# Performance work log

Hardware: AMD Instinct MI355X
Metric: run time of the kernel (lower is better)

Reference implementation:

```python
import jax, jax.numpy as jnp
import numpy as np
import math

B = 65536
N_NUM = 64; N_CAT = 16; CAT_SIZE = 1000; EMB = 16
ND = 64; NA = 64; OUT = ND + NA; NSTEPS = 5; GAMMA = 1.5
NFEAT = N_NUM + N_CAT * EMB          # 320
NGROUPS = N_NUM + N_CAT              # 80
GROUP_IDX = np.repeat(np.arange(NGROUPS), [1] * N_NUM + [EMB] * N_CAT)  # len 320
RES_SCALE = math.sqrt(0.5)
BN_EPS = 1e-5


def setup_inputs() -> dict:
    keys = iter(jax.random.split(jax.random.key(0), 64))
    def rn(shape, std):
        return jax.random.normal(next(keys), shape, jnp.float32) * std
    def mk_bn(c, lead=()):
        # stacked (scale, bias, running_mean, running_var) along axis -2
        s = 1.0 + 0.05 * jax.random.normal(next(keys), (*lead, c), jnp.float32)
        b = 0.05 * jax.random.normal(next(keys), (*lead, c), jnp.float32)
        m = 0.05 * jax.random.normal(next(keys), (*lead, c), jnp.float32)
        v = 1.0 + 0.1 * jax.random.uniform(next(keys), (*lead, c), dtype=jnp.float32)
        return jnp.stack([s, b, m, v], axis=-2)
    inp = {}
    inp["x_num"] = jax.random.normal(next(keys), (B, N_NUM), jnp.float32)
    inp["x_cat"] = jax.random.randint(next(keys), (B, N_CAT), 0, CAT_SIZE)
    inp["emb_W"] = rn((N_CAT, CAT_SIZE, EMB), 0.1)
    inp["in_bn"] = mk_bn(NFEAT)
    inp["sh_W0"] = rn((NFEAT, 2 * OUT), 1.0 / math.sqrt(NFEAT))
    inp["sh_b0"] = jnp.zeros((2 * OUT,), jnp.float32)
    inp["sh_bn0"] = mk_bn(2 * OUT)
    inp["sh_W1"] = rn((OUT, 2 * OUT), 1.0 / math.sqrt(OUT))
    inp["sh_b1"] = jnp.zeros((2 * OUT,), jnp.float32)
    inp["sh_bn1"] = mk_bn(2 * OUT)
    inp["init_W"] = rn((2, OUT, 2 * OUT), 1.0 / math.sqrt(OUT))
    inp["init_b"] = jnp.zeros((2, 2 * OUT), jnp.float32)
    inp["init_bn"] = mk_bn(2 * OUT, (2,))
    inp["step_W"] = rn((NSTEPS, 2, OUT, 2 * OUT), 1.0 / math.sqrt(OUT))
    inp["step_b"] = jnp.zeros((NSTEPS, 2, 2 * OUT), jnp.float32)
    inp["step_bn"] = mk_bn(2 * OUT, (NSTEPS, 2))
    inp["att_W"] = rn((NSTEPS, NA, NGROUPS), 1.0 / math.sqrt(NA))
    inp["att_b"] = jnp.zeros((NSTEPS, NGROUPS), jnp.float32)
    inp["att_bn"] = mk_bn(NGROUPS, (NSTEPS,))
    inp["out_W"] = rn((ND, 1), 1.0 / math.sqrt(ND))
    inp["out_b"] = jnp.zeros((1,), jnp.float32)
    return inp


def bn_apply(x, p):
    s, b, m, v = p  # each [C]
    return (x - m) * jax.lax.rsqrt(v + BN_EPS) * s + b


def glu_layer(x, W, b, bn):
    h = bn_apply(x @ W + b, bn)          # [B, 2*OUT]
    o, g = jnp.split(h, 2, axis=1)
    return o * jax.nn.sigmoid(g)


def glu_block(x, W, b, bn):
    y = glu_layer(x, W, b, bn)
    return (x + y) * RES_SCALE if x.shape == y.shape else y


def sparsemax(z):
    # along axis=1; Martins & Astudillo 2016
    zs = -jnp.sort(-z, axis=1)
    cs = jnp.cumsum(zs, axis=1)
    r = jnp.arange(1, z.shape[1] + 1, dtype=z.dtype)
    support = (1.0 + r * zs) > cs
    k = jnp.maximum(support.sum(axis=1, keepdims=True), 1)
    cs_k = jnp.take_along_axis(cs, k - 1, axis=1)
    tau = (cs_k - 1.0) / k.astype(z.dtype)
    return jnp.maximum(z - tau, 0.0)


def _forward(x_num, x_cat, emb_W, in_bn, sh_W0, sh_b0, sh_bn0, sh_W1, sh_b1, sh_bn1,
             init_W, init_b, init_bn, step_W, step_b, step_bn, att_W, att_b, att_bn,
             out_W, out_b):
    # categorical embeddings: [B, N_CAT, EMB] -> [B, N_CAT*EMB]
    emb = emb_W[np.arange(N_CAT)[None, :], x_cat].reshape(x_cat.shape[0], -1)
    x = jnp.concatenate([x_num, emb], axis=1)  # [B, NFEAT]
    x = bn_apply(x, in_bn)

    def ft_shared(h):
        h = glu_block(h, sh_W0, sh_b0, sh_bn0)   # 320 -> 128, no residual
        return glu_block(h, sh_W1, sh_b1, sh_bn1)  # residual

    def ft_indep(h, W, b, bn):
        for i in range(W.shape[0]):
            h = glu_block(h, W[i], b[i], bn[i])
        return h

    out0 = ft_indep(ft_shared(x), init_W, init_b, init_bn)
    a = out0[:, ND:]
    prior = jnp.ones((x.shape[0], NGROUPS), x.dtype)
    decision_sum = jnp.zeros((x.shape[0], ND), x.dtype)
    for step in range(NSTEPS):
        logits = bn_apply(a @ att_W[step] + att_b[step], att_bn[step]) * prior
        mask_group = sparsemax(logits)           # [B, NGROUPS]
        prior = prior * (GAMMA - mask_group)
        mask = mask_group[:, GROUP_IDX]          # [B, NFEAT] (repeat_interleave)
        out = ft_indep(ft_shared(mask * x), step_W[step], step_b[step], step_bn[step])
        d, a = out[:, :ND], out[:, ND:]
        decision_sum = decision_sum + jax.nn.relu(d)
    return decision_sum @ out_W + out_b          # [B, 1]


def reference(x_num, x_cat, emb_W, in_bn, sh_W0, sh_b0, sh_bn0, sh_W1, sh_b1, sh_bn1,
              init_W, init_b, init_bn, step_W, step_b, step_bn, att_W, att_b, att_bn,
              out_W, out_b):
    return _forward(x_num, x_cat, emb_W, in_bn, sh_W0, sh_b0, sh_bn0, sh_W1, sh_b1,
                    sh_bn1, init_W, init_b, init_bn, step_W, step_b, step_bn,
                    att_W, att_b, att_bn, out_W, out_b)
```

## Files before the change

### kernel.cpp

```cpp
#include <hip/hip_runtime.h>
#include <math.h>
#include <stdint.h>

typedef _Float16 half_t;
typedef _Float16 half8 __attribute__((ext_vector_type(8)));
typedef __fp16 fp16x2 __attribute__((ext_vector_type(2)));
typedef float floatx4 __attribute__((ext_vector_type(4)));
typedef float floatx16 __attribute__((ext_vector_type(16)));

constexpr float BN_EPS_C = 1e-5f;
constexpr float RES_SCALE_C = 0.70710678118654752f;
constexpr float GAMMA_C = 1.5f;
#define B_TOT 65536

__device__ __forceinline__ uint32_t pack2(float y) {
    const half_t h = (half_t)y;
    const half_t l = (half_t)(y - (float)h);
    union { half_t f; unsigned short u; } a, b; a.f = h; b.f = l;
    return (uint32_t)a.u | ((uint32_t)b.u << 16);
}
__device__ __forceinline__ void unpack2(uint32_t v, half_t& h, half_t& l) {
    union { unsigned short u; half_t f; } a, b;
    a.u = (unsigned short)(v & 0xffffu); b.u = (unsigned short)(v >> 16);
    h = a.f; l = b.f;
}
__device__ __forceinline__ void split_pair(float y0, float y1, half_t& h0, half_t& l0, half_t& h1, half_t& l1) {
    fp16x2 hh = __builtin_amdgcn_cvt_pkrtz(y0, y1);
    fp16x2 ll = __builtin_amdgcn_cvt_pkrtz(y0 - (float)hh.x, y1 - (float)hh.y);
    h0 = (half_t)hh.x; l0 = (half_t)ll.x; h1 = (half_t)hh.y; l1 = (half_t)ll.y;
}
__device__ __forceinline__ void pack2_pair(float y0, float y1, uint32_t& w0, uint32_t& w1) {
    fp16x2 hh = __builtin_amdgcn_cvt_pkrtz(y0, y1);
    fp16x2 ll = __builtin_amdgcn_cvt_pkrtz(y0 - (float)hh.x, y1 - (float)hh.y);
    const uint32_t hb = __builtin_bit_cast(uint32_t, hh);
    const uint32_t lb = __builtin_bit_cast(uint32_t, ll);
    w0 = (hb & 0xffffu) | (lb << 16);
    w1 = (hb >> 16) | (lb & 0xffff0000u);
}

__global__ void wsplit_kernel(const float* __restrict__ sh_W0, const float* __restrict__ sh_W1,
                              const float* __restrict__ init_W, const float* __restrict__ step_W,
                              half_t* __restrict__ Wh, half_t* __restrict__ Wl)
{
    const int b = blockIdx.x, n = threadIdx.x;
    const float* src; int k; size_t base;
    if (b < 320)      { src = sh_W0;           k = b;       base = 0; }
    else if (b < 448) { src = sh_W1;           k = b - 320; base = 81920; }
    else if (b < 576) { src = init_W;          k = b - 448; base = 114688; }
    else if (b < 704) { src = init_W + 32768;  k = b - 576; base = 147456; }
    else {
        int j = (b - 704) >> 7; k = (b - 704) & 127;
        src = step_W + (size_t)j * 32768; base = 180224 + (size_t)j * 32768;
    }
    const float v = src[k * 256 + n];
    const half_t hi = (half_t)v;
    const half_t lo = (half_t)(v - (float)hi);
    const size_t idx = base + (size_t)(((k >> 3) * 256 + n) * 8 + (k & 7));
    Wh[idx] = hi; Wl[idx] = lo;
}

__global__ void wsplit_att_kernel(const float* __restrict__ att_W,
                                  half_t* __restrict__ aWh, half_t* __restrict__ aWl)
{
    const int b = blockIdx.x;
    const int n = threadIdx.x;
    const int step = b >> 6, k = b & 63;
    const float v = att_W[(size_t)b * 80 + n];
    const half_t h = (half_t)v;
    const half_t l = (half_t)(v - (float)h);
    const size_t idx = (size_t)step * 5120 + (size_t)(((k >> 3) * 80 + n) * 8 + (k & 7));
    aWh[idx] = h; aWl[idx] = l;
}

__global__ void embed_bn_kernel(const float* __restrict__ x_num, const int* __restrict__ x_cat,
                                const float* __restrict__ emb_W, const float* __restrict__ in_bn,
                                uint32_t* __restrict__ xp)
{
    const int idx = blockIdx.x * 256 + threadIdx.x;
    const int s = idx / 320, j = idx - s * 320;
    float v;
    if (j < 64) v = x_num[(size_t)s * 64 + j];
    else {
        const int c = (j - 64) >> 4, e = (j - 64) & 15;
        v = emb_W[(size_t)(c * 1000 + x_cat[(size_t)s * 16 + c]) * 16 + e];
    }
    const float val = (v - in_bn[640 + j]) * (in_bn[j] * __frsqrt_rn(in_bn[960 + j] + BN_EPS_C)) + in_bn[320 + j];
    xp[idx] = pack2(val);
}

__device__ __forceinline__ void bn_fold(const float* __restrict__ bn, const float* __restrict__ bias,
                                        int c, float& sc, float& sh)
{
    sc = bn[c] * __frsqrt_rn(bn[768 + c] + BN_EPS_C);
    sh = fmaf(bias[c] - bn[512 + c], sc, bn[256 + c]);
}

__device__ __forceinline__ float glu_val(float accO, float accG,
                                         float sc_o, float sh_o, float sc_g, float sh_g)
{
    const float o = fmaf(accO, sc_o, sh_o);
    const float g = fmaf(accG, sc_g, sh_g);
    const float e = __expf(-g);
    return o * __builtin_amdgcn_rcpf(1.f + e);
}

#define MFMA32(A, B, C) C = __builtin_amdgcn_mfma_f32_32x32x16_f16(A, B, C, 0, 0, 0)
#define MFMA16(A, B, C) C = __builtin_amdgcn_mfma_f32_16x16x32_f16(A, B, C, 0, 0, 0)

__device__ __forceinline__ void layer_accum(const half_t (*H_h)[136], const half_t (*H_l)[136],
                                            const half_t* __restrict__ Wh, const half_t* __restrict__ Wl,
                                            size_t off, int n32, int k8, int no, int rot,
                                            floatx16* accO, floatx16* accG)
{
#pragma unroll 2
    for (int s = 0; s < 8; ++s) {
        const int sl8 = (s + rot) & 7;
        const int kq = sl8 * 2 + k8;
        const size_t wo = off + (size_t)(kq * 256 + no + n32) * 8;
        const half8 bo_h = *(const half8*)(Wh + wo);
        const half8 bo_l = *(const half8*)(Wl + wo);
        const half8 bg_h = *(const half8*)(Wh + wo + 1024);
        const half8 bg_l = *(const half8*)(Wl + wo + 1024);
#pragma unroll
        for (int mt = 0; mt < 4; ++mt) {
            const half8 a_h = *(const half8*)&H_h[mt * 32 + n32][sl8 * 16 + k8 * 8];
            const half8 a_l = *(const half8*)&H_l[mt * 32 + n32][sl8 * 16 + k8 * 8];
            MFMA32(a_h, bo_h, accO[mt]); MFMA32(a_h, bg_h, accG[mt]);
            MFMA32(a_l, bo_h, accO[mt]); MFMA32(a_l, bg_h, accG[mt]);
            MFMA32(a_h, bo_l, accO[mt]); MFMA32(a_h, bg_l, accG[mt]);
        }
    }
}

template<bool MASK>
__global__ __launch_bounds__(256, 2)
void ft_chain(const uint32_t* __restrict__ xp, uint32_t* __restrict__ avp,
              const half_t* __restrict__ Wh, const half_t* __restrict__ Wl,
              const half_t* __restrict__ aWh, const half_t* __restrict__ aWl,
              const float* __restrict__ att_b, const float* __restrict__ att_bn,
              float* __restrict__ prior,
              const float* __restrict__ b1, const float* __restrict__ bn1,
              const float* __restrict__ b2, const float* __restrict__ bn2,
              const float* __restrict__ b3, const float* __restrict__ bn3,
              const float* __restrict__ b4, const float* __restrict__ bn4,
              size_t w3_off, size_t w4_off,
              float* __restrict__ ds, int wmode_last, int step)
{
    __shared__ __align__(16) char smem[79872];
    float    (*mgs)[84]  = (float    (*)[84])smem;
    half_t   (*As_h)[72] = (half_t   (*)[72])(smem + 43008);
    half_t   (*As_l)[72] = (half_t   (*)[72])(smem + 61440);
    uint32_t (*Apk)[68]  = (uint32_t (*)[68])(smem + 43008);
    half_t   (*H_h)[136] = (half_t   (*)[136])smem;
    half_t   (*H_l)[136] = (half_t   (*)[136])(smem + 34816);

    const int t = threadIdx.x;
    const int s0 = blockIdx.x * 128;
    const int w = t >> 6, lane = t & 63;
    const int n32 = lane & 31, k8 = lane >> 5;
    const int quad = lane >> 4, l16 = lane & 15;
    const int no = 32 * w;
    const int half_id = (blockIdx.x >> 8) & 1;
    const int row = t >> 1, k0 = (t & 1) * 32;

    if (MASK) {
        {
            const uint4* src = (const uint4*)(avp + (size_t)(s0 + row) * 64 + k0);
            uint4* dst = (uint4*)&Apk[row][k0];
#pragma unroll
            for (int q = 0; q < 8; ++q) dst[q] = src[q];
        }
        __syncthreads();
        floatx4 zacc[2][5];
#pragma unroll
        for (int mt = 0; mt < 2; ++mt)
#pragma unroll
            for (int nt = 0; nt < 5; ++nt) zacc[mt][nt] = (floatx4){0.f, 0.f, 0.f, 0.f};
#pragma unroll
        for (int kc = 0; kc < 64; kc += 32) {
            half8 a_h[2], a_l[2];
#pragma unroll
            for (int mt = 0; mt < 2; ++mt) {
                uint32_t wv[8];
                *(uint4*)&wv[0] = *(const uint4*)&Apk[w * 32 + mt * 16 + l16][kc + quad * 8];
                *(uint4*)&wv[4] = *(const uint4*)&Apk[w * 32 + mt * 16 + l16][kc + quad * 8 + 4];
#pragma unroll
                for (int j = 0; j < 8; ++j) { half_t h, l; unpack2(wv[j], h, l); a_h[mt][j] = h; a_l[mt][j] = l; }
            }
            const int kq = (kc >> 3) + quad;
#pragma unroll
            for (int nt = 0; nt < 5; ++nt) {
                const size_t wi = (size_t)(kq * 80 + nt * 16 + l16) * 8;
                const half8 b_h = *(const half8*)(aWh + wi);
                const half8 b_l = *(const half8*)(aWl + wi);
#pragma unroll
                for (int mt = 0; mt < 2; ++mt) {
                    MFMA16(a_h[mt], b_h, zacc[mt][nt]);
                    MFMA16(a_l[mt], b_h, zacc[mt][nt]);
                    MFMA16(a_h[mt], b_l, zacc[mt][nt]);
                }
            }
        }
        float preg[2][5][4];
#pragma unroll
        for (int nt = 0; nt < 5; ++nt) {
            const int c = nt * 16 + l16;
            const float sc = att_bn[c] * __frsqrt_rn(att_bn[240 + c] + BN_EPS_C);
            const float sh = fmaf(att_b[c] - att_bn[160 + c], sc, att_bn[80 + c]);
#pragma unroll
            for (int mt = 0; mt < 2; ++mt)
#pragma unroll
                for (int r = 0; r < 4; ++r) {
                    const int sl = w * 32 + mt * 16 + quad * 4 + r;
                    const float pr = (step == 0) ? 1.f : prior[(size_t)(s0 + sl) * 80 + c];
                    preg[mt][nt][r] = pr;
                    mgs[sl][c] = fmaf(zacc[mt][nt][r], sc, sh) * pr;
                }
        }
        __syncthreads();
        {
            const int samp = row, j0 = (t & 1) * 40;
            float zj[40], zmax = -1e30f;
#pragma unroll
            for (int j = 0; j < 40; ++j) { zj[j] = mgs[samp][j0 + j]; zmax = fmaxf(zmax, zj[j]); }
            zmax = fmaxf(zmax, __shfl_xor(zmax, 1));
            float lo = zmax - 1.f, hi = zmax;
#pragma unroll 1
            for (int it = 0; it < 16; ++it) {
                const float mid = 0.5f * (lo + hi);
                float ssum = 0.f;
#pragma unroll
                for (int j = 0; j < 40; ++j) ssum += fmaxf(zj[j] - mid, 0.f);
                ssum += __shfl_xor(ssum, 1);
                if (ssum >= 1.f) lo = mid; else hi = mid;
            }
            const float tau = 0.5f * (lo + hi);
#pragma unroll
            for (int j = 0; j < 40; ++j) mgs[samp][j0 + j] = fmaxf(zj[j] - tau, 0.f);
        }
        __syncthreads();
#pragma unroll
        for (int nt = 0; nt < 5; ++nt) {
            const int c = nt * 16 + l16;
#pragma unroll
            for (int mt = 0; mt < 2; ++mt)
#pragma unroll
                for (int r = 0; r < 4; ++r) {
                    const int sl = w * 32 + mt * 16 + quad * 4 + r;
                    prior[(size_t)(s0 + sl) * 80 + c] = preg[mt][nt][r] * (GAMMA_C - mgs[sl][c]);
                }
        }
    }

    floatx16 accO[4], accG[4];
#pragma unroll
    for (int i = 0; i < 4; ++i) { accO[i] = (floatx16)(0.f); accG[i] = (floatx16)(0.f); }

    const uint32_t* arow = xp + (size_t)(s0 + row) * 320 + k0;
    uint32_t pfw[32];
    int ic = half_id * 2;
#pragma unroll
    for (int q = 0; q < 8; ++q)
        *(uint4*)&pfw[q * 4] = *(const uint4*)(arow + ic * 64 + q * 4);

#pragma unroll 1
    for (int i = 0; i < 5; ++i) {
        __syncthreads();
        {
            const int kb = ic * 64 + k0;
            float mA = 1.f, mB = 1.f;
            if (MASK && ic != 0) {
                mA = mgs[row][64 + ((kb - 64) >> 4)];
                mB = mgs[row][64 + ((kb - 48) >> 4)];
            }
#pragma unroll
            for (int q = 0; q < 4; ++q) {
                half8 hh, ll;
                if (MASK && ic == 0) {
                    const float4 m0q = *(const float4*)&mgs[row][kb + q * 8];
                    const float4 m1q = *(const float4*)&mgs[row][kb + q * 8 + 4];
                    const float mm[8] = {m0q.x, m0q.y, m0q.z, m0q.w, m1q.x, m1q.y, m1q.z, m1q.w};
#pragma unroll
                    for (int j = 0; j < 8; ++j) {
                        half_t h, l; unpack2(pfw[q * 8 + j], h, l);
                        const float v = ((float)h + (float)l) * mm[j];
                        const half_t nh = (half_t)v;
                        hh[j] = nh; ll[j] = (half_t)(v - (float)nh);
                    }
                } else if (MASK) {
                    const float m = (q < 2) ? mA : mB;
#pragma unroll
                    for (int j = 0; j < 8; ++j) {
                        half_t h, l; unpack2(pfw[q * 8 + j], h, l);
                        const float v = ((float)h + (float)l) * m;
                        const half_t nh = (half_t)v;
                        hh[j] = nh; ll[j] = (half_t)(v - (float)nh);
                    }
                } else {
#pragma unroll
                    for (int j = 0; j < 8; ++j) { half_t h, l; unpack2(pfw[q * 8 + j], h, l); hh[j] = h; ll[j] = l; }
                }
                *(half8*)&As_h[row][k0 + q * 8] = hh;
                *(half8*)&As_l[row][k0 + q * 8] = ll;
            }
        }
        __syncthreads();
        const int icn = (ic + 1 == 5) ? 0 : ic + 1;
        if (i < 4) {
#pragma unroll
            for (int q = 0; q < 8; ++q)
                *(uint4*)&pfw[q * 4] = *(const uint4*)(arow + icn * 64 + q * 4);
        }
#pragma unroll
        for (int sl4 = 0; sl4 < 4; ++sl4) {
            const int kq = ic * 8 + sl4 * 2 + k8;
            const size_t wo = (size_t)(kq * 256 + no + n32) * 8;
            const half8 bo_h = *(const half8*)(Wh + wo);
            const half8 bo_l = *(const half8*)(Wl + wo);
            const half8 bg_h = *(const half8*)(Wh + wo + 1024);
            const half8 bg_l = *(const half8*)(Wl + wo + 1024);
#pragma unroll
            for (int mt = 0; mt < 4; ++mt) {
                const half8 a_h = *(const half8*)&As_h[mt * 32 + n32][sl4 * 16 + k8 * 8];
                const half8 a_l = *(const half8*)&As_l[mt * 32 + n32][sl4 * 16 + k8 * 8];
                MFMA32(a_h, bo_h, accO[mt]); MFMA32(a_h, bg_h, accG[mt]);
                MFMA32(a_l, bo_h, accO[mt]); MFMA32(a_l, bg_h, accG[mt]);
                MFMA32(a_h, bo_l, accO[mt]); MFMA32(a_h, bg_l, accG[mt]);
            }
        }
        ic = icn;
    }
    __syncthreads();

    {
        const int c = no + n32;
        float sc_o, sh_o, sc_g, sh_g;
        bn_fold(bn1, b1, c, sc_o, sh_o);
        bn_fold(bn1, b1, c + 128, sc_g, sh_g);
#pragma unroll
        for (int mt = 0; mt < 4; ++mt)
#pragma unroll
            for (int q = 0; q < 4; ++q)
#pragma unroll
                for (int rp = 0; rp < 2; ++rp) {
                    const int r0 = q * 4 + rp * 2;
                    const int sl = mt * 32 + rp * 2 + 8 * q + 4 * k8;
                    const float y0 = glu_val(accO[mt][r0],     accG[mt][r0],     sc_o, sh_o, sc_g, sh_g);
                    const float y1 = glu_val(accO[mt][r0 + 1], accG[mt][r0 + 1], sc_o, sh_o, sc_g, sh_g);
                    half_t h0, l0, h1, l1;
                    split_pair(y0, y1, h0, l0, h1, l1);
                    H_h[sl][c] = h0; H_l[sl][c] = l0;
                    H_h[sl + 1][c] = h1; H_l[sl + 1][c] = l1;
                }
    }
    __syncthreads();

#pragma unroll 1
    for (int layer = 0; layer < 2; ++layer) {
        const float* bb = layer ? b3 : b2;
        const float* bn = layer ? bn3 : bn2;
        const size_t off = layer ? w3_off : (size_t)81920;
#pragma unroll
        for (int i = 0; i < 4; ++i) { accO[i] = (floatx16)(0.f); accG[i] = (floatx16)(0.f); }
        layer_accum(H_h, H_l, Wh, Wl, off, n32, k8, no, half_id * 4, accO, accG);
        __syncthreads();
        {
            const int c = no + n32;
            float sc_o, sh_o, sc_g, sh_g;
            bn_fold(bn, bb, c, sc_o, sh_o);
            bn_fold(bn, bb, c + 128, sc_g, sh_g);
#pragma unroll
            for (int mt = 0; mt < 4; ++mt)
#pragma unroll
                for (int q = 0; q < 4; ++q)
#pragma unroll
                    for (int rp = 0; rp < 2; ++rp) {
                        const int r0 = q * 4 + rp * 2;
                        const int sl = mt * 32 + rp * 2 + 8 * q + 4 * k8;
                        const float res0 = (float)H_h[sl][c] + (float)H_l[sl][c];
                        const float res1 = (float)H_h[sl + 1][c] + (float)H_l[sl + 1][c];
                        const float y0 = (glu_val(accO[mt][r0],     accG[mt][r0],     sc_o, sh_o, sc_g, sh_g) + res0) * RES_SCALE_C;
                        const float y1 = (glu_val(accO[mt][r0 + 1], accG[mt][r0 + 1], sc_o, sh_o, sc_g, sh_g) + res1) * RES_SCALE_C;
                        half_t h0, l0, h1, l1;
                        split_pair(y0, y1, h0, l0, h1, l1);
                        H_h[sl][c] = h0; H_l[sl][c] = l0;
                        H_h[sl + 1][c] = h1; H_l[sl + 1][c] = l1;
                    }
        }
        __syncthreads();
    }

#pragma unroll
    for (int i = 0; i < 4; ++i) { accO[i] = (floatx16)(0.f); accG[i] = (floatx16)(0.f); }
    layer_accum(H_h, H_l, Wh, Wl, w4_off, n32, k8, no, half_id * 4, accO, accG);
    {
        const int c = no + n32;
        float sc_o, sh_o, sc_g, sh_g;
        bn_fold(bn4, b4, c, sc_o, sh_o);
        bn_fold(bn4, b4, c + 128, sc_g, sh_g);
        if (w < 2) {
            if (wmode_last != 1) {
#pragma unroll
                for (int mt = 0; mt < 4; ++mt)
#pragma unroll
                    for (int reg = 0; reg < 16; ++reg) {
                        const int sl = mt * 32 + (reg & 3) + 8 * (reg >> 2) + 4 * k8;
                        const float res = (float)H_h[sl][c] + (float)H_l[sl][c];
                        const float y = (glu_val(accO[mt][reg], accG[mt][reg], sc_o, sh_o, sc_g, sh_g) + res) * RES_SCALE_C;
                        const float d = fmaxf(y, 0.f);
                        float* dp = ds + (size_t)(s0 + sl) * 64 + c;
                        *dp = (wmode_last == 2) ? d : (*dp + d);
                    }
            }
        } else {
#pragma unroll
            for (int mt = 0; mt < 4; ++mt)
#pragma unroll
                for (int q = 0; q < 4; ++q)
#pragma unroll
                    for (int rp = 0; rp < 2; ++rp) {
                        const int r0 = q * 4 + rp * 2;
                        const int sl = mt * 32 + rp * 2 + 8 * q + 4 * k8;
                        const float res0 = (float)H_h[sl][c] + (float)H_l[sl][c];
                        const float res1 = (float)H_h[sl + 1][c] + (float)H_l[sl + 1][c];
                        const float y0 = (glu_val(accO[mt][r0],     accG[mt][r0],     sc_o, sh_o, sc_g, sh_g) + res0) * RES_SCALE_C;
                        const float y1 = (glu_val(accO[mt][r0 + 1], accG[mt][r0 + 1], sc_o, sh_o, sc_g, sh_g) + res1) * RES_SCALE_C;
                        uint32_t w0, w1;
                        pack2_pair(y0, y1, w0, w1);
                        avp[(size_t)(s0 + sl) * 64 + (c - 64)] = w0;
                        avp[(size_t)(s0 + sl + 1) * 64 + (c - 64)] = w1;
                    }
        }
    }
}

__global__ void final_kernel(const float* __restrict__ dsum, const float* __restrict__ out_W,
                             const float* __restrict__ out_b, float* __restrict__ out)
{
    const int s = blockIdx.x * 256 + threadIdx.x;
    float acc = out_b[0];
    const float4* dp = (const float4*)(dsum + (size_t)s * 64);
    const float4* wp = (const float4*)out_W;
#pragma unroll
    for (int q = 0; q < 16; ++q) {
        const float4 d = dp[q];
        const float4 ww = wp[q];
        acc += d.x * ww.x + d.y * ww.y + d.z * ww.z + d.w * ww.w;
    }
    out[s] = acc;
}

extern "C" void kernel_launch(void* const* d_in, const int* in_sizes, int n_in,
                              void* d_out, int out_size, void* d_ws, size_t ws_size,
                              hipStream_t stream)
{
    const float* x_num  = (const float*)d_in[0];
    const int*   x_cat  = (const int*)d_in[1];
    const float* emb_W  = (const float*)d_in[2];
    const float* in_bn  = (const float*)d_in[3];
    const float* sh_W0  = (const float*)d_in[4];
    const float* sh_b0  = (const float*)d_in[5];
    const float* sh_bn0 = (const float*)d_in[6];
    const float* sh_W1  = (const float*)d_in[7];
    const float* sh_b1  = (const float*)d_in[8];
    const float* sh_bn1 = (const float*)d_in[9];
    const float* init_W = (const float*)d_in[10];
    const float* init_b = (const float*)d_in[11];
    const float* init_bn= (const float*)d_in[12];
    const float* step_W = (const float*)d_in[13];
    const float* step_b = (const float*)d_in[14];
    const float* step_bn= (const float*)d_in[15];
    const float* att_W  = (const float*)d_in[16];
    const float* att_b  = (const float*)d_in[17];
    const float* att_bn = (const float*)d_in[18];
    const float* out_W  = (const float*)d_in[19];
    const float* out_b  = (const float*)d_in[20];

    const size_t B = B_TOT;
    char* p = (char*)d_ws;
    uint32_t* xp  = (uint32_t*)p;  p += B * 320 * 4;
    uint32_t* avp = (uint32_t*)p;  p += B * 64 * 4;
    half_t* Wh    = (half_t*)p;    p += 507904 * 2;
    half_t* Wl    = (half_t*)p;    p += 507904 * 2;
    half_t* aWh   = (half_t*)p;    p += 25600 * 2;
    half_t* aWl   = (half_t*)p;    p += 25600 * 2;
    float* pri    = (float*)p;     p += B * 80 * 4;
    float* ds     = (float*)p;     p += B * 64 * 4;

    wsplit_kernel<<<1984, 256, 0, stream>>>(sh_W0, sh_W1, init_W, step_W, Wh, Wl);
    wsplit_att_kernel<<<320, 80, 0, stream>>>(att_W, aWh, aWl);
    embed_bn_kernel<<<(B_TOT * 320) / 256, 256, 0, stream>>>(x_num, x_cat, emb_W, in_bn, xp);

    const int GB = B_TOT / 128;
    ft_chain<false><<<GB, 256, 0, stream>>>(xp, avp, Wh, Wl,
                                            nullptr, nullptr, nullptr, nullptr, nullptr,
                                            sh_b0, sh_bn0, sh_b1, sh_bn1,
                                            init_b, init_bn, init_b + 256, init_bn + 1024,
                                            (size_t)114688, (size_t)147456, ds, 1, 0);
    for (int st = 0; st < 5; ++st) {
        const size_t w3 = 180224 + (size_t)(st * 2 + 0) * 32768;
        const size_t w4 = 180224 + (size_t)(st * 2 + 1) * 32768;
        ft_chain<true><<<GB, 256, 0, stream>>>(xp, avp, Wh, Wl,
                                               aWh + st * 5120, aWl + st * 5120,
                                               att_b + st * 80, att_bn + st * 320, pri,
                                               sh_b0, sh_bn0, sh_b1, sh_bn1,
                                               step_b + (st * 2 + 0) * 256, step_bn + (st * 2 + 0) * 1024,
                                               step_b + (st * 2 + 1) * 256, step_bn + (st * 2 + 1) * 1024,
                                               w3, w4, ds, st == 0 ? 2 : 3, st);
    }
    final_kernel<<<B_TOT / 256, 256, 0, stream>>>(ds, out_W, out_b, (float*)d_out);
}
```

Before: 781.6 us.

## Split each 128-sample tile across 8 waves instead of 4

The block grows from 256 to 512 threads. Each wave now owns a 64-row half of the M dimension rather than all 128 rows, which halves the per-wave accumulator tiles. The attention matmul, sparsemax (4 lanes per sample) and staging loads are redistributed to match. This lowers per-thread register pressure and adds more waves to hide latency, at the cost of each B fragment from global memory being loaded by twice as many waves, with extra shuffles and redundant weight traffic.

```diff
diff --git a/kernel.cpp b/kernel.cpp
--- a/kernel.cpp
+++ b/kernel.cpp
@@ -109,7 +109,7 @@
 
 __device__ __forceinline__ void layer_accum(const half_t (*H_h)[136], const half_t (*H_l)[136],
                                             const half_t* __restrict__ Wh, const half_t* __restrict__ Wl,
-                                            size_t off, int n32, int k8, int no, int rot,
+                                            size_t off, int n32, int k8, int no, int m0, int rot,
                                             floatx16* accO, floatx16* accG)
 {
 #pragma unroll 2
@@ -122,9 +122,9 @@
         const half8 bg_h = *(const half8*)(Wh + wo + 1024);
         const half8 bg_l = *(const half8*)(Wl + wo + 1024);
 #pragma unroll
-        for (int mt = 0; mt < 4; ++mt) {
-            const half8 a_h = *(const half8*)&H_h[mt * 32 + n32][sl8 * 16 + k8 * 8];
-            const half8 a_l = *(const half8*)&H_l[mt * 32 + n32][sl8 * 16 + k8 * 8];
+        for (int mt = 0; mt < 2; ++mt) {
+            const half8 a_h = *(const half8*)&H_h[m0 + mt * 32 + n32][sl8 * 16 + k8 * 8];
+            const half8 a_l = *(const half8*)&H_l[m0 + mt * 32 + n32][sl8 * 16 + k8 * 8];
             MFMA32(a_h, bo_h, accO[mt]); MFMA32(a_h, bg_h, accG[mt]);
             MFMA32(a_l, bo_h, accO[mt]); MFMA32(a_l, bg_h, accG[mt]);
             MFMA32(a_h, bo_l, accO[mt]); MFMA32(a_h, bg_l, accG[mt]);
@@ -133,7 +133,7 @@
 }
 
 template<bool MASK>
-__global__ __launch_bounds__(256, 2)
+__global__ __launch_bounds__(512, 4)
 void ft_chain(const uint32_t* __restrict__ xp, uint32_t* __restrict__ avp,
               const half_t* __restrict__ Wh, const half_t* __restrict__ Wl,
               const half_t* __restrict__ aWh, const half_t* __restrict__ aWl,
@@ -157,142 +157,127 @@
     const int t = threadIdx.x;
     const int s0 = blockIdx.x * 128;
     const int w = t >> 6, lane = t & 63;
+    const int wq = w & 3, wh = w >> 2;
     const int n32 = lane & 31, k8 = lane >> 5;
     const int quad = lane >> 4, l16 = lane & 15;
-    const int no = 32 * w;
+    const int no = 32 * wq;
+    const int m0 = wh * 64;
     const int half_id = (blockIdx.x >> 8) & 1;
-    const int row = t >> 1, k0 = (t & 1) * 32;
+    const int rowA = t >> 2, kA = (t & 3) * 16;
 
     if (MASK) {
         {
-            const uint4* src = (const uint4*)(avp + (size_t)(s0 + row) * 64 + k0);
-            uint4* dst = (uint4*)&Apk[row][k0];
-#pragma unroll
-            for (int q = 0; q < 8; ++q) dst[q] = src[q];
-        }
-        __syncthreads();
-        floatx4 zacc[2][5];
-#pragma unroll
-        for (int mt = 0; mt < 2; ++mt)
-#pragma unroll
-            for (int nt = 0; nt < 5; ++nt) zacc[mt][nt] = (floatx4){0.f, 0.f, 0.f, 0.f};
+            const uint4* src = (const uint4*)(avp + (size_t)(s0 + rowA) * 64 + kA);
+            uint4* dst = (uint4*)&Apk[rowA][kA];
+#pragma unroll
+            for (int q = 0; q < 4; ++q) dst[q] = src[q];
+        }
+        __syncthreads();
+        floatx4 zacc[5];
+#pragma unroll
+        for (int nt = 0; nt < 5; ++nt) zacc[nt] = (floatx4){0.f, 0.f, 0.f, 0.f};
 #pragma unroll
         for (int kc = 0; kc < 64; kc += 32) {
-            half8 a_h[2], a_l[2];
-#pragma unroll
-            for (int mt = 0; mt < 2; ++mt) {
-                uint32_t wv[8];
-                *(uint4*)&wv[0] = *(const uint4*)&Apk[w * 32 + mt * 16 + l16][kc + quad * 8];
-                *(uint4*)&wv[4] = *(const uint4*)&Apk[w * 32 + mt * 16 + l16][kc + quad * 8 + 4];
-#pragma unroll
-                for (int j = 0; j < 8; ++j) { half_t h, l; unpack2(wv[j], h, l); a_h[mt][j] = h; a_l[mt][j] = l; }
-            }
+            uint32_t wv[8];
+            *(uint4*)&wv[0] = *(const uint4*)&Apk[w * 16 + l16][kc + quad * 8];
+            *(uint4*)&wv[4] = *(const uint4*)&Apk[w * 16 + l16][kc + quad * 8 + 4];
+            half8 a_h, a_l;
+#pragma unroll
+            for (int j = 0; j < 8; ++j) { half_t h, l; unpack2(wv[j], h, l); a_h[j] = h; a_l[j] = l; }
             const int kq = (kc >> 3) + quad;
 #pragma unroll
             for (int nt = 0; nt < 5; ++nt) {
                 const size_t wi = (size_t)(kq * 80 + nt * 16 + l16) * 8;
                 const half8 b_h = *(const half8*)(aWh + wi);
                 const half8 b_l = *(const half8*)(aWl + wi);
-#pragma unroll
-                for (int mt = 0; mt < 2; ++mt) {
-                    MFMA16(a_h[mt], b_h, zacc[mt][nt]);
-                    MFMA16(a_l[mt], b_h, zacc[mt][nt]);
-                    MFMA16(a_h[mt], b_l, zacc[mt][nt]);
-                }
-            }
-        }
-        float preg[2][5][4];
+                MFMA16(a_h, b_h, zacc[nt]);
+                MFMA16(a_l, b_h, zacc[nt]);
+                MFMA16(a_h, b_l, zacc[nt]);
+            }
+        }
+        float preg[5][4];
 #pragma unroll
         for (int nt = 0; nt < 5; ++nt) {
             const int c = nt * 16 + l16;
             const float sc = att_bn[c] * __frsqrt_rn(att_bn[240 + c] + BN_EPS_C);
             const float sh = fmaf(att_b[c] - att_bn[160 + c], sc, att_bn[80 + c]);
 #pragma unroll
-            for (int mt = 0; mt < 2; ++mt)
-#pragma unroll
-                for (int r = 0; r < 4; ++r) {
-                    const int sl = w * 32 + mt * 16 + quad * 4 + r;
-                    const float pr = (step == 0) ? 1.f : prior[(size_t)(s0 + sl) * 80 + c];
-                    preg[mt][nt][r] = pr;
-                    mgs[sl][c] = fmaf(zacc[mt][nt][r], sc, sh) * pr;
-                }
+            for (int r = 0; r < 4; ++r) {
+                const int sl = w * 16 + quad * 4 + r;
+                const float pr = (step == 0) ? 1.f : prior[(size_t)(s0 + sl) * 80 + c];
+                preg[nt][r] = pr;
+                mgs[sl][c] = fmaf(zacc[nt][r], sc, sh) * pr;
+            }
         }
         __syncthreads();
         {
-            const int samp = row, j0 = (t & 1) * 40;
-            float zj[40], zmax = -1e30f;
-#pragma unroll
-            for (int j = 0; j < 40; ++j) { zj[j] = mgs[samp][j0 + j]; zmax = fmaxf(zmax, zj[j]); }
+            const int samp = rowA, j0 = (t & 3) * 20;
+            float zj[20], zmax = -1e30f;
+#pragma unroll
+            for (int j = 0; j < 20; ++j) { zj[j] = mgs[samp][j0 + j]; zmax = fmaxf(zmax, zj[j]); }
             zmax = fmaxf(zmax, __shfl_xor(zmax, 1));
+            zmax = fmaxf(zmax, __shfl_xor(zmax, 2));
             float lo = zmax - 1.f, hi = zmax;
 #pragma unroll 1
             for (int it = 0; it < 16; ++it) {
                 const float mid = 0.5f * (lo + hi);
                 float ssum = 0.f;
 #pragma unroll
-                for (int j = 0; j < 40; ++j) ssum += fmaxf(zj[j] - mid, 0.f);
+                for (int j = 0; j < 20; ++j) ssum += fmaxf(zj[j] - mid, 0.f);
                 ssum += __shfl_xor(ssum, 1);
+                ssum += __shfl_xor(ssum, 2);
                 if (ssum >= 1.f) lo = mid; else hi = mid;
             }
             const float tau = 0.5f * (lo + hi);
 #pragma unroll
-            for (int j = 0; j < 40; ++j) mgs[samp][j0 + j] = fmaxf(zj[j] - tau, 0.f);
+            for (int j = 0; j < 20; ++j) mgs[samp][j0 + j] = fmaxf(zj[j] - tau, 0.f);
         }
         __syncthreads();
 #pragma unroll
         for (int nt = 0; nt < 5; ++nt) {
             const int c = nt * 16 + l16;
 #pragma unroll
-            for (int mt = 0; mt < 2; ++mt)
-#pragma unroll
-                for (int r = 0; r < 4; ++r) {
-                    const int sl = w * 32 + mt * 16 + quad * 4 + r;
-                    prior[(size_t)(s0 + sl) * 80 + c] = preg[mt][nt][r] * (GAMMA_C - mgs[sl][c]);
-                }
-        }
-    }
-
-    floatx16 accO[4], accG[4];
-#pragma unroll
-    for (int i = 0; i < 4; ++i) { accO[i] = (floatx16)(0.f); accG[i] = (floatx16)(0.f); }
-
-    const uint32_t* arow = xp + (size_t)(s0 + row) * 320 + k0;
-    uint32_t pfw[32];
+            for (int r = 0; r < 4; ++r) {
+                const int sl = w * 16 + quad * 4 + r;
+                prior[(size_t)(s0 + sl) * 80 + c] = preg[nt][r] * (GAMMA_C - mgs[sl][c]);
+            }
+        }
+    }
+
+    floatx16 accO[2], accG[2];
+#pragma unroll
+    for (int i = 0; i < 2; ++i) { accO[i] = (floatx16)(0.f); accG[i] = (floatx16)(0.f); }
+
+    const uint32_t* arow = xp + (size_t)(s0 + rowA) * 320 + kA;
+    uint32_t pfw[16];
     int ic = half_id * 2;
 #pragma unroll
-    for (int q = 0; q < 8; ++q)
+    for (int q = 0; q < 4; ++q)
         *(uint4*)&pfw[q * 4] = *(const uint4*)(arow + ic * 64 + q * 4);
 
 #pragma unroll 1
     for (int i = 0; i < 5; ++i) {
         __syncthreads();
         {
-            const int kb = ic * 64 + k0;
-            float mA = 1.f, mB = 1.f;
-            if (MASK && ic != 0) {
-                mA = mgs[row][64 + ((kb - 64) >> 4)];
-                mB = mgs[row][64 + ((kb - 48) >> 4)];
-            }
-#pragma unroll
-            for (int q = 0; q < 4; ++q) {
+            const int kb = ic * 64 + kA;
+            float mG = 1.f;
+            if (MASK && ic != 0) mG = mgs[rowA][64 + ((kb - 64) >> 4)];
+#pragma unroll
+            for (int q = 0; q < 2; ++q) {
                 half8 hh, ll;
                 if (MASK && ic == 0) {
-                    const float4 m0q = *(const float4*)&mgs[row][kb + q * 8];
-                    const float4 m1q = *(const float4*)&mgs[row][kb + q * 8 + 4];
-                    const float mm[8] = {m0q.x, m0q.y, m0q.z, m0q.w, m1q.x, m1q.y, m1q.z, m1q.w};
 #pragma unroll
                     for (int j = 0; j < 8; ++j) {
                         half_t h, l; unpack2(pfw[q * 8 + j], h, l);
-                        const float v = ((float)h + (float)l) * mm[j];
+                        const float v = ((float)h + (float)l) * mgs[rowA][kb + q * 8 + j];
                         const half_t nh = (half_t)v;
                         hh[j] = nh; ll[j] = (half_t)(v - (float)nh);
                     }
                 } else if (MASK) {
-                    const float m = (q < 2) ? mA : mB;
 #pragma unroll
                     for (int j = 0; j < 8; ++j) {
                         half_t h, l; unpack2(pfw[q * 8 + j], h, l);
-                        const float v = ((float)h + (float)l) * m;
+                        const float v = ((float)h + (float)l) * mG;
                         const half_t nh = (half_t)v;
                         hh[j] = nh; ll[j] = (half_t)(v - (float)nh);
                     }
@@ -300,15 +285,15 @@
 #pragma unroll
                     for (int j = 0; j < 8; ++j) { half_t h, l; unpack2(pfw[q * 8 + j], h, l); hh[j] = h; ll[j] = l; }
                 }
-                *(half8*)&As_h[row][k0 + q * 8] = hh;
-                *(half8*)&As_l[row][k0 + q * 8] = ll;
+                *(half8*)&As_h[rowA][kA + q * 8] = hh;
+                *(half8*)&As_l[rowA][kA + q * 8] = ll;
             }
         }
         __syncthreads();
         const int icn = (ic + 1 == 5) ? 0 : ic + 1;
         if (i < 4) {
 #pragma unroll
-            for (int q = 0; q < 8; ++q)
+            for (int q = 0; q < 4; ++q)
                 *(uint4*)&pfw[q * 4] = *(const uint4*)(arow + icn * 64 + q * 4);
         }
 #pragma unroll
@@ -320,9 +305,9 @@
             const half8 bg_h = *(const half8*)(Wh + wo + 1024);
             const half8 bg_l = *(const half8*)(Wl + wo + 1024);
 #pragma unroll
-            for (int mt = 0; mt < 4; ++mt) {
-                const half8 a_h = *(const half8*)&As_h[mt * 32 + n32][sl4 * 16 + k8 * 8];
-                const half8 a_l = *(const half8*)&As_l[mt * 32 + n32][sl4 * 16 + k8 * 8];
+            for (int mt = 0; mt < 2; ++mt) {
+                const half8 a_h = *(const half8*)&As_h[m0 + mt * 32 + n32][sl4 * 16 + k8 * 8];
+                const half8 a_l = *(const half8*)&As_l[m0 + mt * 32 + n32][sl4 * 16 + k8 * 8];
                 MFMA32(a_h, bo_h, accO[mt]); MFMA32(a_h, bg_h, accG[mt]);
                 MFMA32(a_l, bo_h, accO[mt]); MFMA32(a_l, bg_h, accG[mt]);
                 MFMA32(a_h, bo_l, accO[mt]); MFMA32(a_h, bg_l, accG[mt]);
@@ -338,13 +323,13 @@
         bn_fold(bn1, b1, c, sc_o, sh_o);
         bn_fold(bn1, b1, c + 128, sc_g, sh_g);
 #pragma unroll
-        for (int mt = 0; mt < 4; ++mt)
+        for (int mt = 0; mt < 2; ++mt)
 #pragma unroll
             for (int q = 0; q < 4; ++q)
 #pragma unroll
                 for (int rp = 0; rp < 2; ++rp) {
                     const int r0 = q * 4 + rp * 2;
-                    const int sl = mt * 32 + rp * 2 + 8 * q + 4 * k8;
+                    const int sl = m0 + mt * 32 + rp * 2 + 8 * q + 4 * k8;
                     const float y0 = glu_val(accO[mt][r0],     accG[mt][r0],     sc_o, sh_o, sc_g, sh_g);
                     const float y1 = glu_val(accO[mt][r0 + 1], accG[mt][r0 + 1], sc_o, sh_o, sc_g, sh_g);
                     half_t h0, l0, h1, l1;
@@ -361,8 +346,8 @@
         const float* bn = layer ? bn3 : bn2;
         const size_t off = layer ? w3_off : (size_t)81920;
 #pragma unroll
-        for (int i = 0; i < 4; ++i) { accO[i] = (floatx16)(0.f); accG[i] = (floatx16)(0.f); }
-        layer_accum(H_h, H_l, Wh, Wl, off, n32, k8, no, half_id * 4, accO, accG);
+        for (int i = 0; i < 2; ++i) { accO[i] = (floatx16)(0.f); accG[i] = (floatx16)(0.f); }
+        layer_accum(H_h, H_l, Wh, Wl, off, n32, k8, no, m0, half_id * 4, accO, accG);
         __syncthreads();
         {
             const int c = no + n32;
@@ -370,13 +355,13 @@
             bn_fold(bn, bb, c, sc_o, sh_o);
             bn_fold(bn, bb, c + 128, sc_g, sh_g);
 #pragma unroll
-            for (int mt = 0; mt < 4; ++mt)
+            for (int mt = 0; mt < 2; ++mt)
 #pragma unroll
                 for (int q = 0; q < 4; ++q)
 #pragma unroll
                     for (int rp = 0; rp < 2; ++rp) {
                         const int r0 = q * 4 + rp * 2;
-                        const int sl = mt * 32 + rp * 2 + 8 * q + 4 * k8;
+                        const int sl = m0 + mt * 32 + rp * 2 + 8 * q + 4 * k8;
                         const float res0 = (float)H_h[sl][c] + (float)H_l[sl][c];
                         const float res1 = (float)H_h[sl + 1][c] + (float)H_l[sl + 1][c];
                         const float y0 = (glu_val(accO[mt][r0],     accG[mt][r0],     sc_o, sh_o, sc_g, sh_g) + res0) * RES_SCALE_C;
@@ -391,20 +376,20 @@
     }
 
 #pragma unroll
-    for (int i = 0; i < 4; ++i) { accO[i] = (floatx16)(0.f); accG[i] = (floatx16)(0.f); }
-    layer_accum(H_h, H_l, Wh, Wl, w4_off, n32, k8, no, half_id * 4, accO, accG);
+    for (int i = 0; i < 2; ++i) { accO[i] = (floatx16)(0.f); accG[i] = (floatx16)(0.f); }
+    layer_accum(H_h, H_l, Wh, Wl, w4_off, n32, k8, no, m0, half_id * 4, accO, accG);
     {
         const int c = no + n32;
         float sc_o, sh_o, sc_g, sh_g;
         bn_fold(bn4, b4, c, sc_o, sh_o);
         bn_fold(bn4, b4, c + 128, sc_g, sh_g);
-        if (w < 2) {
+        if (wq < 2) {
             if (wmode_last != 1) {
 #pragma unroll
-                for (int mt = 0; mt < 4; ++mt)
+                for (int mt = 0; mt < 2; ++mt)
 #pragma unroll
                     for (int reg = 0; reg < 16; ++reg) {
-                        const int sl = mt * 32 + (reg & 3) + 8 * (reg >> 2) + 4 * k8;
+                        const int sl = m0 + mt * 32 + (reg & 3) + 8 * (reg >> 2) + 4 * k8;
                         const float res = (float)H_h[sl][c] + (float)H_l[sl][c];
                         const float y = (glu_val(accO[mt][reg], accG[mt][reg], sc_o, sh_o, sc_g, sh_g) + res) * RES_SCALE_C;
                         const float d = fmaxf(y, 0.f);
@@ -414,13 +399,13 @@
             }
         } else {
 #pragma unroll
-            for (int mt = 0; mt < 4; ++mt)
+            for (int mt = 0; mt < 2; ++mt)
 #pragma unroll
                 for (int q = 0; q < 4; ++q)
 #pragma unroll
                     for (int rp = 0; rp < 2; ++rp) {
                         const int r0 = q * 4 + rp * 2;
-                        const int sl = mt * 32 + rp * 2 + 8 * q + 4 * k8;
+                        const int sl = m0 + mt * 32 + rp * 2 + 8 * q + 4 * k8;
                         const float res0 = (float)H_h[sl][c] + (float)H_l[sl][c];
                         const float res1 = (float)H_h[sl + 1][c] + (float)H_l[sl + 1][c];
                         const float y0 = (glu_val(accO[mt][r0],     accG[mt][r0],     sc_o, sh_o, sc_g, sh_g) + res0) * RES_SCALE_C;
@@ -492,7 +477,7 @@
     embed_bn_kernel<<<(B_TOT * 320) / 256, 256, 0, stream>>>(x_num, x_cat, emb_W, in_bn, xp);
 
     const int GB = B_TOT / 128;
-    ft_chain<false><<<GB, 256, 0, stream>>>(xp, avp, Wh, Wl,
+    ft_chain<false><<<GB, 512, 0, stream>>>(xp, avp, Wh, Wl,
                                             nullptr, nullptr, nullptr, nullptr, nullptr,
                                             sh_b0, sh_bn0, sh_b1, sh_bn1,
                                             init_b, init_bn, init_b + 256, init_bn + 1024,
@@ -500,7 +485,7 @@
     for (int st = 0; st < 5; ++st) {
         const size_t w3 = 180224 + (size_t)(st * 2 + 0) * 32768;
         const size_t w4 = 180224 + (size_t)(st * 2 + 1) * 32768;
-        ft_chain<true><<<GB, 256, 0, stream>>>(xp, avp, Wh, Wl,
+        ft_chain<true><<<GB, 512, 0, stream>>>(xp, avp, Wh, Wl,
                                                aWh + st * 5120, aWl + st * 5120,
                                                att_b + st * 80, att_bn + st * 320, pri,
                                                sh_b0, sh_bn0, sh_b1, sh_bn1,
```

Measured after the change: 733.3 us. 6.2% less time.
